# Optimization experiments

Hardware: AMD Instinct MI355X
Metric: run time of the kernel (lower is better)

## Reference

```python
import jax, jax.numpy as jnp
import numpy as np

# Production-scale dims (see shape_source)
B, H, W, K, C = 8, 256, 256, 8, 64
N = B * H * W              # packed point count (one point per source pixel)
RADIUS_PX = 1.5            # module init radius (pixels)
IMG = 256                  # image_size
RAD_POW = 2                # opts.model.rad_pow
R_NDC = RADIUS_PX / IMG * 2.0  # radius scaling done inside forward


def setup_inputs() -> dict:
    key = jax.random.key(0)
    k1, k2, k3, k4, k5 = jax.random.split(key, 5)
    # squared NDC distances, in [0, r^2) as the rasterizer would produce
    dist = jax.random.uniform(k1, (B, H, W, K), jnp.float32) * (R_NDC ** RAD_POW)
    z_buf = jax.random.uniform(k2, (B, H, W, K), jnp.float32) * 2.0 - 0.1
    points_idx = jax.random.randint(k3, (B, H, W, K), 0, N)
    empty = jax.random.uniform(k4, (B, H, W, K)) < 0.1
    points_idx = jnp.where(empty, -1, points_idx)
    features = jax.random.normal(k5, (N, C), jnp.float32)  # features_packed()
    return {"dist": dist, "z_buf": z_buf, "points_idx": points_idx,
            "features": features}


def reference(dist, z_buf, points_idx, features):
    # dist, z_buf: [B,H,W,K]; points_idx: int [B,H,W,K]; features: [N,C]
    # dist = dist / radius**rad_pow; alphas = 1 - clamp(dist,1e-3,1)**0.5
    d = dist / (R_NDC ** RAD_POW)
    alphas = 1.0 - jnp.sqrt(jnp.clip(d, 0.001, 1.0))          # [B,H,W,K]
    alphas = jnp.transpose(alphas, (0, 3, 1, 2))               # [B,K,H,W]
    zb = jnp.transpose(z_buf, (0, 3, 1, 2))                    # [B,K,H,W]
    idx = jnp.transpose(points_idx, (0, 3, 1, 2))              # [B,K,H,W]
    alphas = alphas * (zb >= 0)                                # kill empty depth slots
    valid = idx >= 0
    alphas = alphas * valid                                    # kill empty idx slots
    safe_idx = jnp.where(valid, idx, 0)
    # alpha_composite: w_k = a_k * prod_{j<k} (1 - a_j)  (front-to-back)
    transm = jnp.cumprod(1.0 - alphas, axis=1)
    transm = jnp.concatenate([jnp.ones_like(transm[:, :1]), transm[:, :-1]], axis=1)
    w = alphas * transm                                        # [B,K,H,W]
    gathered = features[safe_idx]                              # [B,K,H,W,C]
    out = jnp.einsum('bkhw,bkhwc->bchw', w, gathered)          # [B,C,H,W]
    return out
```

## Files before the change

kernel.cpp:

```cpp
#include <hip/hip_runtime.h>

#define BN 8
#define HN 256
#define WN 256
#define KN 8
#define CN 64
#define R2 0.0001373291015625f
#define NPTS (BN * HN * WN)
#define FELEMS ((size_t)NPTS * CN)

typedef float    vf4 __attribute__((ext_vector_type(4)));
typedef _Float16 vh4 __attribute__((ext_vector_type(4)));
typedef _Float16 vh8 __attribute__((ext_vector_type(8)));

__global__ __launch_bounds__(256) void feat_to_f16_kernel(
    const float* __restrict__ in, _Float16* __restrict__ o)
{
    const size_t i = (((size_t)blockIdx.x << 8) + threadIdx.x) << 3;
    const vf4 a = __builtin_nontemporal_load((const vf4*)(in + i));
    const vf4 b = __builtin_nontemporal_load((const vf4*)(in + i) + 1);
    vh8 h;
    h[0] = (_Float16)a.x; h[1] = (_Float16)a.y; h[2] = (_Float16)a.z; h[3] = (_Float16)a.w;
    h[4] = (_Float16)b.x; h[5] = (_Float16)b.y; h[6] = (_Float16)b.z; h[7] = (_Float16)b.w;
    *(vh8*)(o + i) = h;
}

__global__ __launch_bounds__(256) void rast_blend_f16_kernel(
    const float* __restrict__ dist,
    const float* __restrict__ zbuf,
    const int*   __restrict__ pidx,
    const _Float16* __restrict__ feat,
    float*       __restrict__ out)
{
    __shared__ float s_w[64][9];
    __shared__ int   s_i[64][9];
    __shared__ float s_o[64][65];

    const int t   = threadIdx.x;
    const int pixBase = blockIdx.x << 6;
    const int bh = pixBase >> 8;
    const int w0 = pixBase & 255;

    const int base = pixBase << 3;
    #pragma unroll
    for (int i = 0; i < 2; ++i) {
        const int e = t + (i << 8);
        const float dd = __builtin_nontemporal_load(dist + base + e);
        const float zz = __builtin_nontemporal_load(zbuf + base + e);
        const int   ii = __builtin_nontemporal_load(pidx + base + e);
        float d = dd / R2;
        float a = 1.0f - sqrtf(fminf(fmaxf(d, 0.001f), 1.0f));
        if (zz < 0.0f || ii < 0) a = 0.0f;
        s_w[e >> 3][e & 7] = a;
        s_i[e >> 3][e & 7] = (ii >= 0) ? ii : 0;
    }
    __syncthreads();

    if (t < 64) {
        float tr = 1.0f;
        #pragma unroll
        for (int k = 0; k < KN; ++k) {
            const float a = s_w[t][k];
            s_w[t][k] = a * tr;
            tr *= (1.0f - a);
        }
    }
    __syncthreads();

    const int wv  = t >> 6;
    const int ln  = t & 63;
    const int sub = ln >> 4;
    const int q   = ln & 15;
    #pragma unroll
    for (int it = 0; it < 4; ++it) {
        const int p = (wv << 4) + (it << 2) + sub;

        float wk[KN];
        const vh4* fp[KN];
        #pragma unroll
        for (int k = 0; k < KN; ++k) {
            wk[k] = s_w[p][k];
            fp[k] = (const vh4*)(feat + ((size_t)s_i[p][k] << 6)) + q;
        }
        vh4 f[KN];
        #pragma unroll
        for (int k = 0; k < KN; ++k) f[k] = *fp[k];

        float ax = 0.0f, ay = 0.0f, az = 0.0f, aw = 0.0f;
        #pragma unroll
        for (int k = 0; k < KN; ++k) {
            ax = fmaf(wk[k], (float)f[k][0], ax);
            ay = fmaf(wk[k], (float)f[k][1], ay);
            az = fmaf(wk[k], (float)f[k][2], az);
            aw = fmaf(wk[k], (float)f[k][3], aw);
        }
        const int c0 = q << 2;
        s_o[c0 + 0][p] = ax;
        s_o[c0 + 1][p] = ay;
        s_o[c0 + 2][p] = az;
        s_o[c0 + 3][p] = aw;
    }
    __syncthreads();

    const int b = bh >> 8;
    const int h = bh & 255;
    const size_t outBase = ((size_t)b * CN) * (HN * WN) + (size_t)h * WN + w0;
    #pragma unroll
    for (int cc = 0; cc < 16; ++cc) {
        const int c = (t >> 6) + (cc << 2);
        __builtin_nontemporal_store(s_o[c][ln],
                                    out + outBase + (size_t)c * (HN * WN) + ln);
    }
}

__global__ __launch_bounds__(256) void rast_blend_f32_kernel(
    const float* __restrict__ dist,
    const float* __restrict__ zbuf,
    const int*   __restrict__ pidx,
    const float* __restrict__ feat,
    float*       __restrict__ out)
{
    __shared__ float s_w[64][9];
    __shared__ int   s_i[64][9];
    __shared__ float s_o[64][65];

    const int t   = threadIdx.x;
    const int pixBase = blockIdx.x << 6;
    const int bh = pixBase >> 8;
    const int w0 = pixBase & 255;

    const int base = pixBase << 3;
    #pragma unroll
    for (int i = 0; i < 2; ++i) {
        const int e = t + (i << 8);
        const float dd = __builtin_nontemporal_load(dist + base + e);
        const float zz = __builtin_nontemporal_load(zbuf + base + e);
        const int   ii = __builtin_nontemporal_load(pidx + base + e);
        float d = dd / R2;
        float a = 1.0f - sqrtf(fminf(fmaxf(d, 0.001f), 1.0f));
        if (zz < 0.0f || ii < 0) a = 0.0f;
        s_w[e >> 3][e & 7] = a;
        s_i[e >> 3][e & 7] = (ii >= 0) ? ii : 0;
    }
    __syncthreads();

    if (t < 64) {
        float tr = 1.0f;
        #pragma unroll
        for (int k = 0; k < KN; ++k) {
            const float a = s_w[t][k];
            s_w[t][k] = a * tr;
            tr *= (1.0f - a);
        }
    }
    __syncthreads();

    const int wv  = t >> 6;
    const int ln  = t & 63;
    const int sub = ln >> 4;
    const int q   = ln & 15;
    #pragma unroll
    for (int it = 0; it < 4; ++it) {
        const int p = (wv << 4) + (it << 2) + sub;
        float wk[KN];
        const float4* fp[KN];
        #pragma unroll
        for (int k = 0; k < KN; ++k) {
            wk[k] = s_w[p][k];
            fp[k] = (const float4*)(feat + ((size_t)s_i[p][k] << 6)) + q;
        }
        float4 f[KN];
        #pragma unroll
        for (int k = 0; k < KN; ++k) f[k] = *fp[k];
        float ax = 0.0f, ay = 0.0f, az = 0.0f, aw = 0.0f;
        #pragma unroll
        for (int k = 0; k < KN; ++k) {
            ax = fmaf(wk[k], f[k].x, ax);
            ay = fmaf(wk[k], f[k].y, ay);
            az = fmaf(wk[k], f[k].z, az);
            aw = fmaf(wk[k], f[k].w, aw);
        }
        const int c0 = q << 2;
        s_o[c0 + 0][p] = ax;
        s_o[c0 + 1][p] = ay;
        s_o[c0 + 2][p] = az;
        s_o[c0 + 3][p] = aw;
    }
    __syncthreads();

    const int b = bh >> 8;
    const int h = bh & 255;
    const size_t outBase = ((size_t)b * CN) * (HN * WN) + (size_t)h * WN + w0;
    #pragma unroll
    for (int cc = 0; cc < 16; ++cc) {
        const int c = (t >> 6) + (cc << 2);
        __builtin_nontemporal_store(s_o[c][ln],
                                    out + outBase + (size_t)c * (HN * WN) + ln);
    }
}

extern "C" void kernel_launch(void* const* d_in, const int* in_sizes, int n_in,
                              void* d_out, int out_size, void* d_ws, size_t ws_size,
                              hipStream_t stream) {
    const float* dist = (const float*)d_in[0];
    const float* zbuf = (const float*)d_in[1];
    const int*   pidx = (const int*)d_in[2];
    const float* feat = (const float*)d_in[3];
    float* out = (float*)d_out;

    const int nPix = BN * HN * WN;
    const int grid = nPix / 64;

    if (ws_size >= FELEMS * sizeof(_Float16)) {
        _Float16* wsf = (_Float16*)d_ws;
        const int convBlocks = (int)(FELEMS / 8 / 256);
        feat_to_f16_kernel<<<convBlocks, 256, 0, stream>>>(feat, wsf);
        rast_blend_f16_kernel<<<grid, 256, 0, stream>>>(dist, zbuf, pidx, wsf, out);
    } else {
        rast_blend_f32_kernel<<<grid, 256, 0, stream>>>(dist, zbuf, pidx, feat, out);
    }
}
```

Measured before the change: 318.3 us.

## Pipeline feature gathers, fuse alpha compositing, stage outputs as f16 in LDS

Fuses the per-slot alpha computation and front-to-back compositing into one pass by 64 threads using vector loads, removing a barrier. It double-buffers the random feature gathers so the next pixel's loads overlap the current pixel's FMAs, and raises the occupancy hint. It also stores blended results to LDS as packed f16 to halve shared memory, which adds rounding error to the output. The f16 feature copy now lives in a static device global instead of the workspace, and the f32 fallback is dropped.

```diff
diff --git a/kernel.cpp b/kernel.cpp
--- a/kernel.cpp
+++ b/kernel.cpp
@@ -10,11 +10,14 @@
 #define FELEMS ((size_t)NPTS * CN)
 
 typedef float    vf4 __attribute__((ext_vector_type(4)));
+typedef int      vi4 __attribute__((ext_vector_type(4)));
+typedef _Float16 vh2 __attribute__((ext_vector_type(2)));
 typedef _Float16 vh4 __attribute__((ext_vector_type(4)));
 typedef _Float16 vh8 __attribute__((ext_vector_type(8)));
 
-__global__ __launch_bounds__(256) void feat_to_f16_kernel(
-    const float* __restrict__ in, _Float16* __restrict__ o)
+__device__ _Float16 g_feat[FELEMS];
+
+__global__ __launch_bounds__(256) void feat_to_f16_kernel(const float* __restrict__ in)
 {
     const size_t i = (((size_t)blockIdx.x << 8) + threadIdx.x) << 3;
     const vf4 a = __builtin_nontemporal_load((const vf4*)(in + i));
@@ -22,47 +25,42 @@
     vh8 h;
     h[0] = (_Float16)a.x; h[1] = (_Float16)a.y; h[2] = (_Float16)a.z; h[3] = (_Float16)a.w;
     h[4] = (_Float16)b.x; h[5] = (_Float16)b.y; h[6] = (_Float16)b.z; h[7] = (_Float16)b.w;
-    *(vh8*)(o + i) = h;
+    *(vh8*)(g_feat + i) = h;
 }
 
-__global__ __launch_bounds__(256) void rast_blend_f16_kernel(
+__global__ __launch_bounds__(256, 8) void rast_blend_f16_kernel(
     const float* __restrict__ dist,
     const float* __restrict__ zbuf,
     const int*   __restrict__ pidx,
-    const _Float16* __restrict__ feat,
     float*       __restrict__ out)
 {
-    __shared__ float s_w[64][9];
-    __shared__ int   s_i[64][9];
-    __shared__ float s_o[64][65];
+    __shared__ float    s_w[64][9];
+    __shared__ int      s_i[64][9];
+    __shared__ unsigned s_o2[32][65];
 
-    const int t   = threadIdx.x;
+    const int t       = threadIdx.x;
     const int pixBase = blockIdx.x << 6;
-    const int bh = pixBase >> 8;
-    const int w0 = pixBase & 255;
-
-    const int base = pixBase << 3;
-    #pragma unroll
-    for (int i = 0; i < 2; ++i) {
-        const int e = t + (i << 8);
-        const float dd = __builtin_nontemporal_load(dist + base + e);
-        const float zz = __builtin_nontemporal_load(zbuf + base + e);
-        const int   ii = __builtin_nontemporal_load(pidx + base + e);
-        float d = dd / R2;
-        float a = 1.0f - sqrtf(fminf(fmaxf(d, 0.001f), 1.0f));
-        if (zz < 0.0f || ii < 0) a = 0.0f;
-        s_w[e >> 3][e & 7] = a;
-        s_i[e >> 3][e & 7] = (ii >= 0) ? ii : 0;
-    }
-    __syncthreads();
 
     if (t < 64) {
+        const size_t eb = ((size_t)(pixBase + t)) << 3;
+        const vf4 d0 = __builtin_nontemporal_load((const vf4*)(dist + eb));
+        const vf4 d1 = __builtin_nontemporal_load((const vf4*)(dist + eb) + 1);
+        const vf4 z0 = __builtin_nontemporal_load((const vf4*)(zbuf + eb));
+        const vf4 z1 = __builtin_nontemporal_load((const vf4*)(zbuf + eb) + 1);
+        const vi4 i0 = __builtin_nontemporal_load((const vi4*)(pidx + eb));
+        const vi4 i1 = __builtin_nontemporal_load((const vi4*)(pidx + eb) + 1);
+        const float dd[8] = {d0.x, d0.y, d0.z, d0.w, d1.x, d1.y, d1.z, d1.w};
+        const float zz[8] = {z0.x, z0.y, z0.z, z0.w, z1.x, z1.y, z1.z, z1.w};
+        const int   ii[8] = {i0.x, i0.y, i0.z, i0.w, i1.x, i1.y, i1.z, i1.w};
         float tr = 1.0f;
         #pragma unroll
         for (int k = 0; k < KN; ++k) {
-            const float a = s_w[t][k];
+            const float d = dd[k] / R2;
+            float a = 1.0f - sqrtf(fminf(fmaxf(d, 0.001f), 1.0f));
+            if (zz[k] < 0.0f || ii[k] < 0) a = 0.0f;
             s_w[t][k] = a * tr;
             tr *= (1.0f - a);
+            s_i[t][k] = (ii[k] >= 0) ? ii[k] : 0;
         }
     }
     __syncthreads();
@@ -71,131 +69,58 @@
     const int ln  = t & 63;
     const int sub = ln >> 4;
     const int q   = ln & 15;
-    #pragma unroll
-    for (int it = 0; it < 4; ++it) {
-        const int p = (wv << 4) + (it << 2) + sub;
+    const int p0  = (wv << 4) + sub;
 
-        float wk[KN];
-        const vh4* fp[KN];
-        #pragma unroll
-        for (int k = 0; k < KN; ++k) {
-            wk[k] = s_w[p][k];
-            fp[k] = (const vh4*)(feat + ((size_t)s_i[p][k] << 6)) + q;
-        }
-        vh4 f[KN];
-        #pragma unroll
-        for (int k = 0; k < KN; ++k) f[k] = *fp[k];
+#define GATHER(F, P) do {                                                     \
+    _Pragma("unroll")                                                         \
+    for (int k = 0; k < KN; ++k)                                              \
+        F[k] = *((const vh4*)(g_feat + ((size_t)s_i[(P)][k] << 6)) + q);      \
+} while (0)
 
-        float ax = 0.0f, ay = 0.0f, az = 0.0f, aw = 0.0f;
-        #pragma unroll
-        for (int k = 0; k < KN; ++k) {
-            ax = fmaf(wk[k], (float)f[k][0], ax);
-            ay = fmaf(wk[k], (float)f[k][1], ay);
-            az = fmaf(wk[k], (float)f[k][2], az);
-            aw = fmaf(wk[k], (float)f[k][3], aw);
-        }
-        const int c0 = q << 2;
-        s_o[c0 + 0][p] = ax;
-        s_o[c0 + 1][p] = ay;
-        s_o[c0 + 2][p] = az;
-        s_o[c0 + 3][p] = aw;
-    }
+#define COMPUTE(F, P) do {                                                    \
+    float ax = 0.0f, ay = 0.0f, az = 0.0f, aw = 0.0f;                         \
+    _Pragma("unroll")                                                         \
+    for (int k = 0; k < KN; ++k) {                                            \
+        const float wk = s_w[(P)][k];                                         \
+        ax = fmaf(wk, (float)F[k][0], ax);                                    \
+        ay = fmaf(wk, (float)F[k][1], ay);                                    \
+        az = fmaf(wk, (float)F[k][2], az);                                    \
+        aw = fmaf(wk, (float)F[k][3], aw);                                    \
+    }                                                                         \
+    vh2 h0; h0[0] = (_Float16)ax; h0[1] = (_Float16)ay;                       \
+    vh2 h1; h1[0] = (_Float16)az; h1[1] = (_Float16)aw;                       \
+    s_o2[(q << 1) + 0][(P)] = __builtin_bit_cast(unsigned, h0);               \
+    s_o2[(q << 1) + 1][(P)] = __builtin_bit_cast(unsigned, h1);               \
+} while (0)
+
+    vh4 fA[KN], fB[KN];
+    GATHER(fA, p0);
+    GATHER(fB, p0 + 4);
+    COMPUTE(fA, p0);
+    GATHER(fA, p0 + 8);
+    COMPUTE(fB, p0 + 4);
+    GATHER(fB, p0 + 12);
+    COMPUTE(fA, p0 + 8);
+    COMPUTE(fB, p0 + 12);
+
+#undef GATHER
+#undef COMPUTE
+
     __syncthreads();
 
-    const int b = bh >> 8;
-    const int h = bh & 255;
+    const int bh = pixBase >> 8;
+    const int w0 = pixBase & 255;
+    const int b  = bh >> 8;
+    const int h  = bh & 255;
     const size_t outBase = ((size_t)b * CN) * (HN * WN) + (size_t)h * WN + w0;
     #pragma unroll
-    for (int cc = 0; cc < 16; ++cc) {
-        const int c = (t >> 6) + (cc << 2);
-        __builtin_nontemporal_store(s_o[c][ln],
-                                    out + outBase + (size_t)c * (HN * WN) + ln);
-    }
-}
-
-__global__ __launch_bounds__(256) void rast_blend_f32_kernel(
-    const float* __restrict__ dist,
-    const float* __restrict__ zbuf,
-    const int*   __restrict__ pidx,
-    const float* __restrict__ feat,
-    float*       __restrict__ out)
-{
-    __shared__ float s_w[64][9];
-    __shared__ int   s_i[64][9];
-    __shared__ float s_o[64][65];
-
-    const int t   = threadIdx.x;
-    const int pixBase = blockIdx.x << 6;
-    const int bh = pixBase >> 8;
-    const int w0 = pixBase & 255;
-
-    const int base = pixBase << 3;
-    #pragma unroll
-    for (int i = 0; i < 2; ++i) {
-        const int e = t + (i << 8);
-        const float dd = __builtin_nontemporal_load(dist + base + e);
-        const float zz = __builtin_nontemporal_load(zbuf + base + e);
-        const int   ii = __builtin_nontemporal_load(pidx + base + e);
-        float d = dd / R2;
-        float a = 1.0f - sqrtf(fminf(fmaxf(d, 0.001f), 1.0f));
-        if (zz < 0.0f || ii < 0) a = 0.0f;
-        s_w[e >> 3][e & 7] = a;
-        s_i[e >> 3][e & 7] = (ii >= 0) ? ii : 0;
-    }
-    __syncthreads();
-
-    if (t < 64) {
-        float tr = 1.0f;
-        #pragma unroll
-        for (int k = 0; k < KN; ++k) {
-            const float a = s_w[t][k];
-            s_w[t][k] = a * tr;
-            tr *= (1.0f - a);
-        }
-    }
-    __syncthreads();
-
-    const int wv  = t >> 6;
-    const int ln  = t & 63;
-    const int sub = ln >> 4;
-    const int q   = ln & 15;
-    #pragma unroll
-    for (int it = 0; it < 4; ++it) {
-        const int p = (wv << 4) + (it << 2) + sub;
-        float wk[KN];
-        const float4* fp[KN];
-        #pragma unroll
-        for (int k = 0; k < KN; ++k) {
-            wk[k] = s_w[p][k];
-            fp[k] = (const float4*)(feat + ((size_t)s_i[p][k] << 6)) + q;
-        }
-        float4 f[KN];
-        #pragma unroll
-        for (int k = 0; k < KN; ++k) f[k] = *fp[k];
-        float ax = 0.0f, ay = 0.0f, az = 0.0f, aw = 0.0f;
-        #pragma unroll
-        for (int k = 0; k < KN; ++k) {
-            ax = fmaf(wk[k], f[k].x, ax);
-            ay = fmaf(wk[k], f[k].y, ay);
-            az = fmaf(wk[k], f[k].z, az);
-            aw = fmaf(wk[k], f[k].w, aw);
-        }
-        const int c0 = q << 2;
-        s_o[c0 + 0][p] = ax;
-        s_o[c0 + 1][p] = ay;
-        s_o[c0 + 2][p] = az;
-        s_o[c0 + 3][p] = aw;
-    }
-    __syncthreads();
-
-    const int b = bh >> 8;
-    const int h = bh & 255;
-    const size_t outBase = ((size_t)b * CN) * (HN * WN) + (size_t)h * WN + w0;
-    #pragma unroll
-    for (int cc = 0; cc < 16; ++cc) {
-        const int c = (t >> 6) + (cc << 2);
-        __builtin_nontemporal_store(s_o[c][ln],
-                                    out + outBase + (size_t)c * (HN * WN) + ln);
+    for (int cc = 0; cc < 8; ++cc) {
+        const int cw = wv + (cc << 2);
+        const vh2 hv = __builtin_bit_cast(vh2, s_o2[cw][ln]);
+        __builtin_nontemporal_store((float)hv[0],
+            out + outBase + (size_t)(2 * cw + 0) * (HN * WN) + ln);
+        __builtin_nontemporal_store((float)hv[1],
+            out + outBase + (size_t)(2 * cw + 1) * (HN * WN) + ln);
     }
 }
 
@@ -208,15 +133,12 @@
     const float* feat = (const float*)d_in[3];
     float* out = (float*)d_out;
 
+    (void)d_ws; (void)ws_size;
+
     const int nPix = BN * HN * WN;
     const int grid = nPix / 64;
 
-    if (ws_size >= FELEMS * sizeof(_Float16)) {
-        _Float16* wsf = (_Float16*)d_ws;
-        const int convBlocks = (int)(FELEMS / 8 / 256);
-        feat_to_f16_kernel<<<convBlocks, 256, 0, stream>>>(feat, wsf);
-        rast_blend_f16_kernel<<<grid, 256, 0, stream>>>(dist, zbuf, pidx, wsf, out);
-    } else {
-        rast_blend_f32_kernel<<<grid, 256, 0, stream>>>(dist, zbuf, pidx, feat, out);
-    }
+    const int convBlocks = (int)(FELEMS / 8 / 256);
+    feat_to_f16_kernel<<<convBlocks, 256, 0, stream>>>(feat);
+    rast_blend_f16_kernel<<<grid, 256, 0, stream>>>(dist, zbuf, pidx, out);
 }
```

New measurement: 379.0 us. 19.0% more time.

## Widen f16 feature gathers, fuse alpha prologue, stage output as packed halves

Applied to the files above, without the earlier changes.

The f16 blend kernel now has one wavefront load each pixel's 8 dist/z/idx values as vectors and compute alphas plus transmittance in a single pass, which removes a barrier. Each lane gathers 16-byte (8-half) feature chunks, and two pixels' gathers are issued before any compute so more memory requests are in flight. Results are staged in LDS as packed half pairs, which halves shared memory use, and launch bounds request higher occupancy. The cost is that outputs are rounded to fp16 before the final store, adding precision loss, and only 64 of 256 threads do the prologue work.

```diff
diff --git a/kernel.cpp b/kernel.cpp
--- a/kernel.cpp
+++ b/kernel.cpp
@@ -10,8 +10,10 @@
 #define FELEMS ((size_t)NPTS * CN)
 
 typedef float    vf4 __attribute__((ext_vector_type(4)));
-typedef _Float16 vh4 __attribute__((ext_vector_type(4)));
+typedef int      vi4 __attribute__((ext_vector_type(4)));
+typedef _Float16 vh2 __attribute__((ext_vector_type(2)));
 typedef _Float16 vh8 __attribute__((ext_vector_type(8)));
+
 
 __global__ __launch_bounds__(256) void feat_to_f16_kernel(
     const float* __restrict__ in, _Float16* __restrict__ o)
@@ -25,11 +27,104 @@
     *(vh8*)(o + i) = h;
 }
 
-__global__ __launch_bounds__(256) void rast_blend_f16_kernel(
+__global__ __launch_bounds__(256, 8) void rast_blend_f16_kernel(
     const float* __restrict__ dist,
     const float* __restrict__ zbuf,
     const int*   __restrict__ pidx,
     const _Float16* __restrict__ feat,
+    float*       __restrict__ out)
+{
+    __shared__ float    s_w[64][9];
+    __shared__ int      s_i[64][9];
+    __shared__ unsigned s_o2[32][65];
+
+    const int t       = threadIdx.x;
+    const int pixBase = blockIdx.x << 6;
+
+    if (t < 64) {
+        const size_t eb = ((size_t)(pixBase + t)) << 3;
+        const vf4 d0 = __builtin_nontemporal_load((const vf4*)(dist + eb));
+        const vf4 d1 = __builtin_nontemporal_load((const vf4*)(dist + eb) + 1);
+        const vf4 z0 = __builtin_nontemporal_load((const vf4*)(zbuf + eb));
+        const vf4 z1 = __builtin_nontemporal_load((const vf4*)(zbuf + eb) + 1);
+        const vi4 i0 = __builtin_nontemporal_load((const vi4*)(pidx + eb));
+        const vi4 i1 = __builtin_nontemporal_load((const vi4*)(pidx + eb) + 1);
+        const float dd[8] = {d0.x, d0.y, d0.z, d0.w, d1.x, d1.y, d1.z, d1.w};
+        const float zz[8] = {z0.x, z0.y, z0.z, z0.w, z1.x, z1.y, z1.z, z1.w};
+        const int   ii[8] = {i0.x, i0.y, i0.z, i0.w, i1.x, i1.y, i1.z, i1.w};
+        float tr = 1.0f;
+        #pragma unroll
+        for (int k = 0; k < KN; ++k) {
+            const float d = dd[k] / R2;
+            float a = 1.0f - sqrtf(fminf(fmaxf(d, 0.001f), 1.0f));
+            if (zz[k] < 0.0f || ii[k] < 0) a = 0.0f;
+            s_w[t][k] = a * tr;
+            tr *= (1.0f - a);
+            s_i[t][k] = (ii[k] >= 0) ? ii[k] : 0;
+        }
+    }
+    __syncthreads();
+
+    const int wv  = t >> 6;
+    const int ln  = t & 63;
+    const int sub = ln >> 3;
+    const int o   = ln & 7;
+    const int p0  = (wv << 4) + sub;
+
+#define GATHER8(F, P) do {                                                    \
+    _Pragma("unroll")                                                         \
+    for (int k = 0; k < KN; ++k)                                              \
+        F[k] = *((const vh8*)(feat + ((size_t)s_i[(P)][k] << 6)) + o);        \
+} while (0)
+
+#define COMPUTE8(F, P) do {                                                   \
+    float acc[8] = {0,0,0,0,0,0,0,0};                                         \
+    _Pragma("unroll")                                                         \
+    for (int k = 0; k < KN; ++k) {                                            \
+        const float wk = s_w[(P)][k];                                         \
+        _Pragma("unroll")                                                     \
+        for (int j = 0; j < 8; ++j)                                           \
+            acc[j] = fmaf(wk, (float)F[k][j], acc[j]);                        \
+    }                                                                         \
+    _Pragma("unroll")                                                         \
+    for (int j2 = 0; j2 < 4; ++j2) {                                          \
+        vh2 hp; hp[0] = (_Float16)acc[2*j2]; hp[1] = (_Float16)acc[2*j2+1];   \
+        s_o2[(o << 2) + j2][(P)] = __builtin_bit_cast(unsigned, hp);          \
+    }                                                                         \
+} while (0)
+
+    vh8 fA[KN], fB[KN];
+    GATHER8(fA, p0);
+    GATHER8(fB, p0 + 8);
+    COMPUTE8(fA, p0);
+    COMPUTE8(fB, p0 + 8);
+
+#undef GATHER8
+#undef COMPUTE8
+
+    __syncthreads();
+
+    const int bh = pixBase >> 8;
+    const int w0 = pixBase & 255;
+    const int b  = bh >> 8;
+    const int h  = bh & 255;
+    const size_t outBase = ((size_t)b * CN) * (HN * WN) + (size_t)h * WN + w0;
+    #pragma unroll
+    for (int cc = 0; cc < 8; ++cc) {
+        const int cw = wv + (cc << 2);
+        const vh2 hv = __builtin_bit_cast(vh2, s_o2[cw][ln]);
+        __builtin_nontemporal_store((float)hv[0],
+            out + outBase + (size_t)(2 * cw + 0) * (HN * WN) + ln);
+        __builtin_nontemporal_store((float)hv[1],
+            out + outBase + (size_t)(2 * cw + 1) * (HN * WN) + ln);
+    }
+}
+
+__global__ __launch_bounds__(256) void rast_blend_f32_kernel(
+    const float* __restrict__ dist,
+    const float* __restrict__ zbuf,
+    const int*   __restrict__ pidx,
+    const float* __restrict__ feat,
     float*       __restrict__ out)
 {
     __shared__ float s_w[64][9];
@@ -74,94 +169,6 @@
     #pragma unroll
     for (int it = 0; it < 4; ++it) {
         const int p = (wv << 4) + (it << 2) + sub;
-
-        float wk[KN];
-        const vh4* fp[KN];
-        #pragma unroll
-        for (int k = 0; k < KN; ++k) {
-            wk[k] = s_w[p][k];
-            fp[k] = (const vh4*)(feat + ((size_t)s_i[p][k] << 6)) + q;
-        }
-        vh4 f[KN];
-        #pragma unroll
-        for (int k = 0; k < KN; ++k) f[k] = *fp[k];
-
-        float ax = 0.0f, ay = 0.0f, az = 0.0f, aw = 0.0f;
-        #pragma unroll
-        for (int k = 0; k < KN; ++k) {
-            ax = fmaf(wk[k], (float)f[k][0], ax);
-            ay = fmaf(wk[k], (float)f[k][1], ay);
-            az = fmaf(wk[k], (float)f[k][2], az);
-            aw = fmaf(wk[k], (float)f[k][3], aw);
-        }
-        const int c0 = q << 2;
-        s_o[c0 + 0][p] = ax;
-        s_o[c0 + 1][p] = ay;
-        s_o[c0 + 2][p] = az;
-        s_o[c0 + 3][p] = aw;
-    }
-    __syncthreads();
-
-    const int b = bh >> 8;
-    const int h = bh & 255;
-    const size_t outBase = ((size_t)b * CN) * (HN * WN) + (size_t)h * WN + w0;
-    #pragma unroll
-    for (int cc = 0; cc < 16; ++cc) {
-        const int c = (t >> 6) + (cc << 2);
-        __builtin_nontemporal_store(s_o[c][ln],
-                                    out + outBase + (size_t)c * (HN * WN) + ln);
-    }
-}
-
-__global__ __launch_bounds__(256) void rast_blend_f32_kernel(
-    const float* __restrict__ dist,
-    const float* __restrict__ zbuf,
-    const int*   __restrict__ pidx,
-    const float* __restrict__ feat,
-    float*       __restrict__ out)
-{
-    __shared__ float s_w[64][9];
-    __shared__ int   s_i[64][9];
-    __shared__ float s_o[64][65];
-
-    const int t   = threadIdx.x;
-    const int pixBase = blockIdx.x << 6;
-    const int bh = pixBase >> 8;
-    const int w0 = pixBase & 255;
-
-    const int base = pixBase << 3;
-    #pragma unroll
-    for (int i = 0; i < 2; ++i) {
-        const int e = t + (i << 8);
-        const float dd = __builtin_nontemporal_load(dist + base + e);
-        const float zz = __builtin_nontemporal_load(zbuf + base + e);
-        const int   ii = __builtin_nontemporal_load(pidx + base + e);
-        float d = dd / R2;
-        float a = 1.0f - sqrtf(fminf(fmaxf(d, 0.001f), 1.0f));
-        if (zz < 0.0f || ii < 0) a = 0.0f;
-        s_w[e >> 3][e & 7] = a;
-        s_i[e >> 3][e & 7] = (ii >= 0) ? ii : 0;
-    }
-    __syncthreads();
-
-    if (t < 64) {
-        float tr = 1.0f;
-        #pragma unroll
-        for (int k = 0; k < KN; ++k) {
-            const float a = s_w[t][k];
-            s_w[t][k] = a * tr;
-            tr *= (1.0f - a);
-        }
-    }
-    __syncthreads();
-
-    const int wv  = t >> 6;
-    const int ln  = t & 63;
-    const int sub = ln >> 4;
-    const int q   = ln & 15;
-    #pragma unroll
-    for (int it = 0; it < 4; ++it) {
-        const int p = (wv << 4) + (it << 2) + sub;
         float wk[KN];
         const float4* fp[KN];
         #pragma unroll
```

Result: slower. 342.4 us (+7.6%).
